# Optimization experiments

Measured on AMD Instinct MI355X. Metric: run time of the kernel, lower is better.

The kernel has to match this reference:

```python
import jax, jax.numpy as jnp
import numpy as np

BN_EPS = 1e-5


def conv1d_reflect(x, w, dilation, bias=None):
    # x: [N, C_in, L], w: [C_out, C_in, K]; reflect pad preserves length for K=3, pad=dilation
    k = w.shape[-1]
    p = ((k - 1) * dilation + 1) // 2
    xp = jnp.pad(x, ((0, 0), (0, 0), (p, p)), mode='reflect')
    y = jax.lax.conv_general_dilated(
        xp, w, window_strides=(1,), padding='VALID',
        rhs_dilation=(dilation,), dimension_numbers=('NCH', 'OIH', 'NCH'))
    if bias is not None:
        y = y + bias[None, :, None]
    return y


def bn_eval(x, gamma, beta, mean, var):
    inv = gamma / jnp.sqrt(var + BN_EPS)
    return x * inv[None, :, None] + (beta - mean * inv)[None, :, None]


def upsample2_linear(x):
    # F.interpolate(scale_factor=2, mode='linear', align_corners=False)
    L = x.shape[-1]
    src = (jnp.arange(2 * L, dtype=jnp.float32) + 0.5) * 0.5 - 0.5
    src = jnp.maximum(src, 0.0)
    i0 = jnp.floor(src).astype(jnp.int32)
    i1 = jnp.minimum(i0 + 1, L - 1)
    w = (src - i0.astype(jnp.float32)).astype(x.dtype)
    return x[..., i0] * (1.0 - w) + x[..., i1] * w


def setup_inputs() -> dict:
    key = jax.random.key(0)
    ks = jax.random.split(key, 6)
    bt, st, ch, nt = 16, 4, 512, 1024
    fusion = jax.random.normal(ks[0], (bt, st, ch, nt), dtype=jnp.float32)
    targets = jax.random.uniform(ks[1], (bt, 3, 4 * nt, st), dtype=jnp.float32)
    c1, c2 = 256, 32
    w1 = jax.random.normal(ks[2], (c1, ch, 3), dtype=jnp.float32) * 0.05
    w2 = jax.random.normal(ks[3], (c2, c1, 3), dtype=jnp.float32) * 0.05
    w_out = jax.random.normal(ks[4], (3, c2, 3), dtype=jnp.float32) * 0.05
    b_out = jnp.zeros((3,), dtype=jnp.float32)
    return {
        'fusion': fusion, 'targets': targets,
        'w1': w1,
        'bn1_gamma': jnp.ones((c1,), jnp.float32), 'bn1_beta': jnp.zeros((c1,), jnp.float32),
        'bn1_mean': jnp.zeros((c1,), jnp.float32), 'bn1_var': jnp.ones((c1,), jnp.float32),
        'w2': w2,
        'bn2_gamma': jnp.ones((c2,), jnp.float32), 'bn2_beta': jnp.zeros((c2,), jnp.float32),
        'bn2_mean': jnp.zeros((c2,), jnp.float32), 'bn2_var': jnp.ones((c2,), jnp.float32),
        'w_out': w_out, 'b_out': b_out,
    }


def reference(fusion, targets, w1, bn1_gamma, bn1_beta, bn1_mean, bn1_var,
              w2, bn2_gamma, bn2_beta, bn2_mean, bn2_var, w_out, b_out):
    bt, st, ch, nt = fusion.shape
    x = fusion.reshape(bt * st, ch, nt)
    x = jax.nn.relu(bn_eval(conv1d_reflect(x, w1, dilation=8), bn1_gamma, bn1_beta, bn1_mean, bn1_var))
    x = upsample2_linear(x)
    x = jax.nn.relu(bn_eval(conv1d_reflect(x, w2, dilation=16), bn2_gamma, bn2_beta, bn2_mean, bn2_var))
    x = upsample2_linear(x)
    x = conv1d_reflect(x, w_out, dilation=32, bias=b_out)
    x = x.reshape(bt, st, x.shape[1], x.shape[2])
    x = jnp.transpose(x, (0, 2, 3, 1))  # [bt, 3, 4*nt, st]

    # losses: vectorized masked CE (replaces the python double loop)
    logp = jax.nn.log_softmax(x.astype(jnp.float32), axis=1)
    valid = jnp.any(targets != 0, axis=(1, 2))  # [bt, st]
    num = jnp.sum(valid).astype(jnp.float32)
    T = targets.shape[2]
    loss = jnp.sum(-targets * logp) / (num * T)
    return x, loss
```

## Files before the change

### kernel.cpp

```cpp
#include <hip/hip_runtime.h>
#include <hip/hip_bf16.h>

#define DEV static __device__ __forceinline__

typedef short bf16x8_t __attribute__((ext_vector_type(8)));
typedef float f32x4 __attribute__((ext_vector_type(4)));

#define GLDS16(gp, lp) __builtin_amdgcn_global_load_lds( \
    (const __attribute__((address_space(1))) void*)(gp), \
    (__attribute__((address_space(3))) void*)(lp), 16, 0, 0)

DEV int reflect_idx(int q, int L) {
    q = q < 0 ? -q : q;
    q = q >= L ? 2 * L - 2 - q : q;
    return q;
}

DEV unsigned short f2bf(float f) {
    unsigned int b = __float_as_uint(f);
    unsigned int r = (b + 0x7FFFu + ((b >> 16) & 1u)) >> 16;
    return (unsigned short)r;
}
DEV float bf2f(unsigned short u) {
    return __uint_as_float(((unsigned int)u) << 16);
}

__global__ __launch_bounds__(256) void kprep_xt(
        const float* __restrict__ x, const float* __restrict__ w1,
        const float* __restrict__ w2, unsigned short* __restrict__ xb,
        unsigned short* __restrict__ wb, unsigned short* __restrict__ w2b,
        float* lacc, int n0) {
    const int tid = threadIdx.x;

    if (n0 == 0) {
        int bid = (blockIdx.z * gridDim.y + blockIdx.y) * gridDim.x + blockIdx.x;
        int g = bid * 256 + tid;
        if (g < 393216) {
            int kk = g >> 17;
            int rem = g & 131071;
            int co = rem >> 9;
            int ci = rem & 511;
            wb[g] = f2bf(w1[(co * 512 + ci) * 3 + kk]);
        } else if (g < 417792) {
            int j = g - 393216;
            int ci = j & 255;
            int co = (j >> 8) & 31;
            int kk = j >> 13;
            w2b[j] = f2bf(w2[(co * 256 + ci) * 3 + kk]);
        }
        if (g < 128) lacc[g] = 0.0f;
    }

    __shared__ float ls[64][65];
    const int t0 = blockIdx.x * 64, ci0 = blockIdx.y * 64;
    const int n = n0 + blockIdx.z;
    const float* xp = x + ((size_t)n * 512 + ci0) * 1024 + t0;

    float4 v[4];
#pragma unroll
    for (int i = 0; i < 4; ++i) {
        int idx = tid + i * 256;
        int r = idx >> 4, c4 = (idx & 15) * 4;
        v[i] = *(const float4*)(xp + r * 1024 + c4);
    }
#pragma unroll
    for (int i = 0; i < 4; ++i) {
        int idx = tid + i * 256;
        int r = idx >> 4, c4 = (idx & 15) * 4;
        ls[r][c4] = v[i].x; ls[r][c4 + 1] = v[i].y;
        ls[r][c4 + 2] = v[i].z; ls[r][c4 + 3] = v[i].w;
    }
    __syncthreads();
    unsigned short* xo = xb + ((size_t)blockIdx.z * 1024 + t0) * 512 + ci0;
#pragma unroll
    for (int p = 0; p < 2; ++p) {
        int trow = (tid >> 3) + p * 32;
        int cj = (tid & 7) * 8;
        unsigned short pk[8];
#pragma unroll
        for (int j = 0; j < 8; ++j) pk[j] = f2bf(ls[cj + j][trow]);
        *(uint4*)(xo + (size_t)trow * 512 + cj) = *(const uint4*)pk;
    }
}

__global__ __launch_bounds__(256, 4) void k1_mfma(
    const unsigned short* __restrict__ xb, const unsigned short* __restrict__ wb,
    const float* __restrict__ g, const float* __restrict__ be,
    const float* __restrict__ mn, const float* __restrict__ vr,
    unsigned short* __restrict__ y1t, int n0)
{
    const int tid  = threadIdx.x;
    const int lane = tid & 63;
    const int w    = tid >> 6;
    const int tw   = w >> 1;
    const int cw   = w & 1;
    const int tq   = lane & 15;
    const int qd   = lane >> 4;
    const int t0   = (blockIdx.x & 7) * 128;
    const int cb   = blockIdx.x >> 3;
    const int nr   = blockIdx.y;
    const int n    = n0 + nr;

    __shared__ unsigned short smem[17408];

    const int rl0 = tid >> 2;
    const int rl1 = 64 + (tid >> 2);
    const int q0  = (tid & 3) ^ ((rl0 >> 1) & 3);
    const int q1  = (tid & 3) ^ ((rl1 >> 1) & 3);
    const unsigned short* wp0 = wb + (size_t)(cb * 128 + rl0) * 512 + q0 * 8;
    const unsigned short* wp1 = wb + (size_t)(cb * 128 + rl1) * 512 + q1 * 8;

    const unsigned short* xn = xb + (size_t)nr * 1024 * 512;
    const int qA = (tid & 3) ^ ((tid >> 3) & 3);
    int arA[3];
#pragma unroll
    for (int rd = 0; rd < 3; ++rd) {
        int r = rd * 64 + (tid >> 2);
        arA[rd] = reflect_idx(t0 + r - 8, 1024) * 512 + qA * 8;
    }

    const int atom = qd ^ ((tq >> 1) & 3);

    f32x4 acc[4][4];
#pragma unroll
    for (int a = 0; a < 4; ++a)
#pragma unroll
        for (int b = 0; b < 4; ++b) acc[a][b] = (f32x4){0.f, 0.f, 0.f, 0.f};

#define K1A(ch) do { \
    const int ao_ = ((ch) & 1) * 4608; \
    GLDS16(xn + arA[0] + (ch) * 32, &smem[ao_ + tid * 8]); \
    GLDS16(xn + arA[1] + (ch) * 32, &smem[ao_ + 2048 + tid * 8]); \
    if (tid < 64) GLDS16(xn + arA[2] + (ch) * 32, &smem[ao_ + 4096 + tid * 8]); \
} while (0)

#define K1B(i) do { \
    const int kk_ = (i) % 3; const int ch_ = (i) / 3; \
    const int bo_ = 9216 + ((i) & 1) * 4096; \
    GLDS16(wp0 + (size_t)kk_ * 131072 + ch_ * 32, &smem[bo_ + tid * 8]); \
    GLDS16(wp1 + (size_t)kk_ * 131072 + ch_ * 32, &smem[bo_ + 2048 + tid * 8]); \
} while (0)

    K1A(0);
    K1B(0);

#pragma unroll
    for (int c = 0; c < 48; ++c) {
        __syncthreads();
        if (c < 47) K1B(c + 1);
        if ((c % 3) == 2 && c < 45) K1A(c / 3 + 1);
        const int kk = c % 3;
        const int ab = ((c / 3) & 1) * 4608;
        const int bb = 9216 + (c & 1) * 4096;
        bf16x8_t Af[4], Bf[4];
#pragma unroll
        for (int ts = 0; ts < 4; ++ts)
            Af[ts] = *(const bf16x8_t*)&smem[ab + (tw * 64 + ts * 16 + tq + 8 * kk) * 32 + atom * 8];
#pragma unroll
        for (int cs = 0; cs < 4; ++cs)
            Bf[cs] = *(const bf16x8_t*)&smem[bb + (cw * 64 + cs * 16 + tq) * 32 + atom * 8];
#pragma unroll
        for (int ts = 0; ts < 4; ++ts)
#pragma unroll
            for (int cs = 0; cs < 4; ++cs)
                acc[ts][cs] = __builtin_amdgcn_mfma_f32_16x16x32_bf16(
                    Af[ts], Bf[cs], acc[ts][cs], 0, 0, 0);
    }
#undef K1A
#undef K1B

    __syncthreads();
#pragma unroll
    for (int cs = 0; cs < 4; ++cs) {
        int col = cw * 64 + cs * 16 + tq;
        int co  = cb * 128 + col;
        float iv = g[co] / sqrtf(vr[co] + 1e-5f);
        float sh = be[co] - mn[co] * iv;
#pragma unroll
        for (int ts = 0; ts < 4; ++ts)
#pragma unroll
            for (int rg = 0; rg < 4; ++rg)
                smem[(tw * 64 + ts * 16 + qd * 4 + rg) * 136 + col] =
                    f2bf(fmaxf(fmaf(acc[ts][cs][rg], iv, sh), 0.0f));
    }
    __syncthreads();
    const int srow = tid >> 4, sseg = tid & 15;
#pragma unroll
    for (int p = 0; p < 8; ++p) {
        int row = p * 16 + srow;
        unsigned short* yp = y1t + ((size_t)n * 1024 + t0 + row) * 256 + cb * 128 + sseg * 8;
        *(uint4*)yp = *(const uint4*)&smem[row * 136 + sseg * 8];
    }
}

__global__ __launch_bounds__(256, 2) void k2_mfma(
    const unsigned short* __restrict__ y1t, const unsigned short* __restrict__ w2b,
    const float* __restrict__ g, const float* __restrict__ be,
    const float* __restrict__ mn, const float* __restrict__ vr,
    float* __restrict__ y2t)
{
    const int tid  = threadIdx.x;
    const int lane = tid & 63;
    const int w    = tid >> 6;
    const int tq   = lane & 15;
    const int qd   = lane >> 4;
    const int t0   = blockIdx.x * 256;
    const int n    = blockIdx.y;

    __shared__ union SM {
        unsigned short us[2][288 * 40];
        float tr[256 * 36];
    } sm;

    f32x4 acc[4][2];
#pragma unroll
    for (int a = 0; a < 4; ++a)
#pragma unroll
        for (int b = 0; b < 2; ++b) acc[a][b] = (f32x4){0.f, 0.f, 0.f, 0.f};

    const unsigned short* yn = y1t + (size_t)n * 1024 * 256;

    auto stage = [&](int ch, int buf) {
        const int ci0 = ch * 32;
        for (int idx = tid; idx < 1152; idx += 256) {
            int r = idx >> 2, gq = idx & 3;
            int u = reflect_idx(t0 - 16 + r, 2048);
            float src = fmaxf((float)u * 0.5f - 0.25f, 0.0f);
            int i0 = (int)src;
            float wl = src - (float)i0;
            int i1 = i0 + 1 > 1023 ? 1023 : i0 + 1;
            const unsigned short* p0 = yn + (size_t)i0 * 256 + ci0 + gq * 8;
            const unsigned short* p1 = yn + (size_t)i1 * 256 + ci0 + gq * 8;
            uint4 ua = *(const uint4*)p0;
            uint4 ub = *(const uint4*)p1;
            const unsigned short* sa = (const unsigned short*)&ua;
            const unsigned short* sb = (const unsigned short*)&ub;
            unsigned short pk[8];
#pragma unroll
            for (int j = 0; j < 8; ++j) {
                float a = bf2f(sa[j]);
                float b = bf2f(sb[j]);
                pk[j] = f2bf(a + wl * (b - a));
            }
            *(uint4*)&sm.us[buf][r * 40 + gq * 8] = *(const uint4*)pk;
        }
    };

    stage(0, 0);
    for (int ch = 0; ch < 8; ++ch) {
        const int buf = ch & 1;
        __syncthreads();
        if (ch < 7) stage(ch + 1, buf ^ 1);

        const int ci0 = ch * 32;
        bf16x8_t Bf[2][3];
#pragma unroll
        for (int cs = 0; cs < 2; ++cs)
#pragma unroll
            for (int kk = 0; kk < 3; ++kk)
                Bf[cs][kk] = *(const bf16x8_t*)(w2b +
                    ((size_t)(kk * 32 + cs * 16 + tq)) * 256 + ci0 + qd * 8);

        bf16x8_t Af[6];
#pragma unroll
        for (int s = 0; s < 6; ++s)
            Af[s] = *(const bf16x8_t*)&sm.us[buf][(w * 64 + s * 16 + tq) * 40 + qd * 8];

#pragma unroll
        for (int ts = 0; ts < 4; ++ts)
#pragma unroll
            for (int cs = 0; cs < 2; ++cs)
#pragma unroll
                for (int kk = 0; kk < 3; ++kk)
                    acc[ts][cs] = __builtin_amdgcn_mfma_f32_16x16x32_bf16(
                        Af[ts + kk], Bf[cs][kk], acc[ts][cs], 0, 0, 0);
    }

    __syncthreads();
#pragma unroll
    for (int cs = 0; cs < 2; ++cs) {
        int co = cs * 16 + tq;
        float iv = g[co] / sqrtf(vr[co] + 1e-5f);
        float sh = be[co] - mn[co] * iv;
#pragma unroll
        for (int ts = 0; ts < 4; ++ts)
#pragma unroll
            for (int rg = 0; rg < 4; ++rg) {
                int tl = w * 64 + ts * 16 + qd * 4 + rg;
                sm.tr[tl * 36 + co] = fmaxf(fmaf(acc[ts][cs][rg], iv, sh), 0.0f);
            }
    }
    __syncthreads();
    float* yo = y2t + ((size_t)n * 2048 + t0 + tid) * 32;
#pragma unroll
    for (int j = 0; j < 8; ++j)
        *(float4*)(yo + j * 4) = *(const float4*)&sm.tr[tid * 36 + j * 4];
}

__global__ __launch_bounds__(256, 2) void k3_ce(
    const float* __restrict__ y2t, const float* __restrict__ w3,
    const float* __restrict__ bias, const float* __restrict__ tg,
    float* __restrict__ out, float* lacc)
{
    const int tid = threadIdx.x;
    const int t0 = blockIdx.x * 256;
    const int n  = blockIdx.y;

    __shared__ float us[32 * 321];
    __shared__ float wsh[288];
    __shared__ float wsum[4];
    __shared__ int snz[4];

    for (int idx = tid; idx < 288; idx += 256) wsh[idx] = w3[idx];

    const float* yn = y2t + (size_t)n * 2048 * 32;
    for (int idx = tid; idx < 1280; idx += 256) {
        int r = idx >> 2, gq = idx & 3;
        int u = reflect_idx(t0 - 32 + r, 4096);
        float src = fmaxf((float)u * 0.5f - 0.25f, 0.0f);
        int i0 = (int)src;
        float wl = src - (float)i0;
        int i1 = i0 + 1 > 2047 ? 2047 : i0 + 1;
        const float* p0 = yn + (size_t)i0 * 32 + gq * 8;
        const float* p1 = yn + (size_t)i1 * 32 + gq * 8;
        float4 a0 = *(const float4*)p0;
        float4 a1 = *(const float4*)(p0 + 4);
        float4 b0 = *(const float4*)p1;
        float4 b1 = *(const float4*)(p1 + 4);
        float v[8];
        v[0] = a0.x + wl * (b0.x - a0.x); v[1] = a0.y + wl * (b0.y - a0.y);
        v[2] = a0.z + wl * (b0.z - a0.z); v[3] = a0.w + wl * (b0.w - a0.w);
        v[4] = a1.x + wl * (b1.x - a1.x); v[5] = a1.y + wl * (b1.y - a1.y);
        v[6] = a1.z + wl * (b1.z - a1.z); v[7] = a1.w + wl * (b1.w - a1.w);
#pragma unroll
        for (int j = 0; j < 8; ++j)
            us[(gq * 8 + j) * 321 + r] = v[j];
    }
    __syncthreads();

    float a0 = 0.0f, a1 = 0.0f, a2 = 0.0f;
#pragma unroll 8
    for (int ci = 0; ci < 32; ++ci) {
        float x0 = us[ci * 321 + tid];
        float x1 = us[ci * 321 + tid + 32];
        float x2 = us[ci * 321 + tid + 64];
        a0 = fmaf(wsh[(0 * 32 + ci) * 3 + 0], x0, a0);
        a0 = fmaf(wsh[(0 * 32 + ci) * 3 + 1], x1, a0);
        a0 = fmaf(wsh[(0 * 32 + ci) * 3 + 2], x2, a0);
        a1 = fmaf(wsh[(1 * 32 + ci) * 3 + 0], x0, a1);
        a1 = fmaf(wsh[(1 * 32 + ci) * 3 + 1], x1, a1);
        a1 = fmaf(wsh[(1 * 32 + ci) * 3 + 2], x2, a1);
        a2 = fmaf(wsh[(2 * 32 + ci) * 3 + 0], x0, a2);
        a2 = fmaf(wsh[(2 * 32 + ci) * 3 + 1], x1, a2);
        a2 = fmaf(wsh[(2 * 32 + ci) * 3 + 2], x2, a2);
    }
    int b = n >> 2, s = n & 3;
    int t = t0 + tid;
    size_t ob = ((size_t)(b * 3) * 4096 + t) * 4 + s;
    float x0 = a0 + bias[0];
    float x1 = a1 + bias[1];
    float x2 = a2 + bias[2];
    out[ob]         = x0;
    out[ob + 16384] = x1;
    out[ob + 32768] = x2;

    float mx = fmaxf(x0, fmaxf(x1, x2));
    float e0 = expf(x0 - mx), e1 = expf(x1 - mx), e2 = expf(x2 - mx);
    float lse = mx + logf(e0 + e1 + e2);
    float g0 = tg[ob], g1 = tg[ob + 16384], g2 = tg[ob + 32768];
    float v = g0 * (lse - x0) + g1 * (lse - x1) + g2 * (lse - x2);
    bool nz = (g0 != 0.0f) | (g1 != 0.0f) | (g2 != 0.0f);

    for (int off = 32; off > 0; off >>= 1) v += __shfl_down(v, off);
    unsigned long long m = __ballot(nz);
    int lane = tid & 63, wid = tid >> 6;
    if (lane == 0) { wsum[wid] = v; snz[wid] = (m != 0ull); }
    __syncthreads();
    if (tid == 0) {
        atomicAdd(lacc, wsum[0] + wsum[1] + wsum[2] + wsum[3]);
        if (snz[0] | snz[1] | snz[2] | snz[3])
            atomicOr((int*)lacc + 8 + n, 1);
    }
}

__global__ void k4c_final(const float* lacc, float* out) {
    if (threadIdx.x == 0) {
        float sum = lacc[0];
        const int* vf = (const int*)lacc + 8;
        int num = 0;
#pragma unroll
        for (int j = 0; j < 64; ++j) num += (vf[j] != 0);
        out[786432] = sum / ((float)num * 4096.0f);
    }
}

extern "C" void kernel_launch(void* const* d_in, const int* in_sizes, int n_in,
                              void* d_out, int out_size, void* d_ws, size_t ws_size,
                              hipStream_t stream) {
    (void)in_sizes; (void)n_in; (void)out_size;
    const float* fusion  = (const float*)d_in[0];
    const float* targets = (const float*)d_in[1];
    const float* w1  = (const float*)d_in[2];
    const float* g1  = (const float*)d_in[3];
    const float* be1 = (const float*)d_in[4];
    const float* mn1 = (const float*)d_in[5];
    const float* vr1 = (const float*)d_in[6];
    const float* w2  = (const float*)d_in[7];
    const float* g2  = (const float*)d_in[8];
    const float* be2 = (const float*)d_in[9];
    const float* mn2 = (const float*)d_in[10];
    const float* vr2 = (const float*)d_in[11];
    const float* w3  = (const float*)d_in[12];
    const float* b3  = (const float*)d_in[13];
    float* out = (float*)d_out;

    char* ws = (char*)d_ws;
    unsigned short* y1t = (unsigned short*)ws;
    unsigned short* xb  = (unsigned short*)(ws + 33554432);
    float* y2t = (float*)(ws + 33554432);

    const bool single = ws_size >= 101500000ull;
    size_t woff = single ? (33554432ull + 67108864ull) : (33554432ull + 16777216ull);
    unsigned short* wb  = (unsigned short*)(ws + woff);
    unsigned short* w2b = (unsigned short*)(ws + woff + 786432);
    float* lacc = (float*)(ws + woff + 786432 + 49152);

    if (single) {
        kprep_xt<<<dim3(16, 8, 64), 256, 0, stream>>>(fusion, w1, w2, xb, wb, w2b, lacc, 0);
        k1_mfma<<<dim3(16, 64), 256, 0, stream>>>(xb, wb, g1, be1, mn1, vr1, y1t, 0);
    } else {
        for (int r = 0; r < 4; ++r) {
            kprep_xt<<<dim3(16, 8, 16), 256, 0, stream>>>(fusion, w1, w2, xb, wb, w2b, lacc, r * 16);
            k1_mfma<<<dim3(16, 16), 256, 0, stream>>>(xb, wb, g1, be1, mn1, vr1, y1t, r * 16);
        }
    }
    k2_mfma<<<dim3(8, 64), 256, 0, stream>>>(y1t, w2b, g2, be2, mn2, vr2, y2t);
    k3_ce<<<dim3(16, 64), 256, 0, stream>>>(y2t, w3, b3, targets, out, lacc);
    k4c_final<<<1, 64, 0, stream>>>(lacc, out);
}
```

Baseline: 333.5 us.

## Halve k2 time tile, precompute upsample indices in LDS, use packed bf16 convert

The k2 conv kernel now processes 128 time steps per block instead of 256 and launches twice as many blocks, with launch bounds raised to 4 blocks per CU. This is meant to improve occupancy and wave balance across the GPU. Upsample source indices and weights are computed once per block into shared memory rather than recomputed in every staging pass, and bf16 packing uses the hardware v_cvt_pk_bf16_f32 instruction. In exchange, the halo overhead per block grows (160 staged rows for 128 outputs versus 288 for 256), and the weight fragments are reloaded by twice as many blocks.

```diff
diff --git a/kernel.cpp b/kernel.cpp
--- a/kernel.cpp
+++ b/kernel.cpp
@@ -193,7 +193,7 @@
     }
 }
 
-__global__ __launch_bounds__(256, 2) void k2_mfma(
+__global__ __launch_bounds__(256, 4) void k2_mfma(
     const unsigned short* __restrict__ y1t, const unsigned short* __restrict__ w2b,
     const float* __restrict__ g, const float* __restrict__ be,
     const float* __restrict__ mn, const float* __restrict__ vr,
@@ -204,17 +204,33 @@
     const int w    = tid >> 6;
     const int tq   = lane & 15;
     const int qd   = lane >> 4;
-    const int t0   = blockIdx.x * 256;
+    const int t0   = blockIdx.x * 128;
     const int n    = blockIdx.y;
 
     __shared__ union SM {
-        unsigned short us[2][288 * 40];
-        float tr[256 * 36];
+        struct {
+            unsigned short us[2][160 * 40];
+            int   tb0[160];
+            int   tb1[160];
+            float tbw[160];
+        } s;
+        float tr[128 * 36];
     } sm;
 
-    f32x4 acc[4][2];
-#pragma unroll
-    for (int a = 0; a < 4; ++a)
+    if (tid < 160) {
+        int u = reflect_idx(t0 - 16 + tid, 2048);
+        float src = fmaxf((float)u * 0.5f - 0.25f, 0.0f);
+        int i0 = (int)src;
+        float wl = src - (float)i0;
+        int i1 = i0 + 1 > 1023 ? 1023 : i0 + 1;
+        sm.s.tb0[tid] = i0 * 256;
+        sm.s.tb1[tid] = i1 * 256;
+        sm.s.tbw[tid] = wl;
+    }
+
+    f32x4 acc[2][2];
+#pragma unroll
+    for (int a = 0; a < 2; ++a)
 #pragma unroll
         for (int b = 0; b < 2; ++b) acc[a][b] = (f32x4){0.f, 0.f, 0.f, 0.f};
 
@@ -222,30 +238,33 @@
 
     auto stage = [&](int ch, int buf) {
         const int ci0 = ch * 32;
-        for (int idx = tid; idx < 1152; idx += 256) {
+        for (int idx = tid; idx < 640; idx += 256) {
             int r = idx >> 2, gq = idx & 3;
-            int u = reflect_idx(t0 - 16 + r, 2048);
-            float src = fmaxf((float)u * 0.5f - 0.25f, 0.0f);
-            int i0 = (int)src;
-            float wl = src - (float)i0;
-            int i1 = i0 + 1 > 1023 ? 1023 : i0 + 1;
-            const unsigned short* p0 = yn + (size_t)i0 * 256 + ci0 + gq * 8;
-            const unsigned short* p1 = yn + (size_t)i1 * 256 + ci0 + gq * 8;
+            const unsigned short* p0 = yn + sm.s.tb0[r] + ci0 + gq * 8;
+            const unsigned short* p1 = yn + sm.s.tb1[r] + ci0 + gq * 8;
+            float wl = sm.s.tbw[r];
             uint4 ua = *(const uint4*)p0;
             uint4 ub = *(const uint4*)p1;
             const unsigned short* sa = (const unsigned short*)&ua;
             const unsigned short* sb = (const unsigned short*)&ub;
-            unsigned short pk[8];
+            float f[8];
 #pragma unroll
             for (int j = 0; j < 8; ++j) {
                 float a = bf2f(sa[j]);
                 float b = bf2f(sb[j]);
-                pk[j] = f2bf(a + wl * (b - a));
+                f[j] = fmaf(wl, b - a, a);
             }
-            *(uint4*)&sm.us[buf][r * 40 + gq * 8] = *(const uint4*)pk;
+            unsigned int c0, c1, c2, c3;
+            asm("v_cvt_pk_bf16_f32 %0, %1, %2" : "=v"(c0) : "v"(f[0]), "v"(f[1]));
+            asm("v_cvt_pk_bf16_f32 %0, %1, %2" : "=v"(c1) : "v"(f[2]), "v"(f[3]));
+            asm("v_cvt_pk_bf16_f32 %0, %1, %2" : "=v"(c2) : "v"(f[4]), "v"(f[5]));
+            asm("v_cvt_pk_bf16_f32 %0, %1, %2" : "=v"(c3) : "v"(f[6]), "v"(f[7]));
+            uint4 st; st.x = c0; st.y = c1; st.z = c2; st.w = c3;
+            *(uint4*)&sm.s.us[buf][r * 40 + gq * 8] = st;
         }
     };
 
+    __syncthreads();
     stage(0, 0);
     for (int ch = 0; ch < 8; ++ch) {
         const int buf = ch & 1;
@@ -261,13 +280,13 @@
                 Bf[cs][kk] = *(const bf16x8_t*)(w2b +
                     ((size_t)(kk * 32 + cs * 16 + tq)) * 256 + ci0 + qd * 8);
 
-        bf16x8_t Af[6];
-#pragma unroll
-        for (int s = 0; s < 6; ++s)
-            Af[s] = *(const bf16x8_t*)&sm.us[buf][(w * 64 + s * 16 + tq) * 40 + qd * 8];
-
-#pragma unroll
-        for (int ts = 0; ts < 4; ++ts)
+        bf16x8_t Af[4];
+#pragma unroll
+        for (int s = 0; s < 4; ++s)
+            Af[s] = *(const bf16x8_t*)&sm.s.us[buf][(w * 32 + s * 16 + tq) * 40 + qd * 8];
+
+#pragma unroll
+        for (int ts = 0; ts < 2; ++ts)
 #pragma unroll
             for (int cs = 0; cs < 2; ++cs)
 #pragma unroll
@@ -283,18 +302,18 @@
         float iv = g[co] / sqrtf(vr[co] + 1e-5f);
         float sh = be[co] - mn[co] * iv;
 #pragma unroll
-        for (int ts = 0; ts < 4; ++ts)
+        for (int ts = 0; ts < 2; ++ts)
 #pragma unroll
             for (int rg = 0; rg < 4; ++rg) {
-                int tl = w * 64 + ts * 16 + qd * 4 + rg;
+                int tl = w * 32 + ts * 16 + qd * 4 + rg;
                 sm.tr[tl * 36 + co] = fmaxf(fmaf(acc[ts][cs][rg], iv, sh), 0.0f);
             }
     }
     __syncthreads();
-    float* yo = y2t + ((size_t)n * 2048 + t0 + tid) * 32;
-#pragma unroll
-    for (int j = 0; j < 8; ++j)
-        *(float4*)(yo + j * 4) = *(const float4*)&sm.tr[tid * 36 + j * 4];
+    float* yo = y2t + ((size_t)n * 2048 + t0 + (tid >> 1)) * 32 + (tid & 1) * 16;
+#pragma unroll
+    for (int j = 0; j < 4; ++j)
+        *(float4*)(yo + j * 4) = *(const float4*)&sm.tr[(tid >> 1) * 36 + (tid & 1) * 16 + j * 4];
 }
 
 __global__ __launch_bounds__(256, 2) void k3_ce(
@@ -434,7 +453,7 @@
             k1_mfma<<<dim3(16, 16), 256, 0, stream>>>(xb, wb, g1, be1, mn1, vr1, y1t, r * 16);
         }
     }
-    k2_mfma<<<dim3(8, 64), 256, 0, stream>>>(y1t, w2b, g2, be2, mn2, vr2, y2t);
+    k2_mfma<<<dim3(16, 64), 256, 0, stream>>>(y1t, w2b, g2, be2, mn2, vr2, y2t);
     k3_ce<<<dim3(16, 64), 256, 0, stream>>>(y2t, w3, b3, targets, out, lacc);
     k4c_final<<<1, 64, 0, stream>>>(lacc, out);
 }
```

Measured after the change: 340.6 us. +2.1%, slower.
